# Kernel tuning notes

Hardware: AMD Instinct MI355X
Metric: run time of the kernel (lower is better)

Reference implementation:

```python
import jax, jax.numpy as jnp
import numpy as np

N, IN_CH, OUT_CH, E = 16384, 512, 512, 8


def setup_inputs() -> dict:
    key = jax.random.key(0)
    k1, k2, k3, k4 = jax.random.split(key, 4)
    x = jax.random.normal(k1, (N, IN_CH), dtype=jnp.float32)
    coefficients = jax.random.uniform(k2, (N, E), dtype=jnp.float32)
    # kaiming-uniform-ish init: bound = 1/sqrt(fan_in)
    bound = 1.0 / np.sqrt(IN_CH)
    weight = jax.random.uniform(k3, (E, OUT_CH, IN_CH), minval=-bound, maxval=bound, dtype=jnp.float32)
    bias = jax.random.uniform(k4, (E, OUT_CH), minval=-bound, maxval=bound, dtype=jnp.float32)
    return {"x": x, "coefficients": coefficients, "weight": weight, "bias": bias}


def reference(x, coefficients, weight, bias):
    # Original: mixed_weight = einsum('bc,cmn->bmn', coef, W); out = baddbmm(mixed_bias, mixed_weight, x)
    # Equivalent (by bilinearity) without materializing the (N,out,in) tensor:
    # per-expert matvec combined with coefficients in one einsum.
    out = jnp.einsum('ne,eoi,ni->no', coefficients, weight, x)
    out = out + coefficients @ bias  # (N,E) @ (E,out) -> (N,out)
    return out
```

## Files before the change

### kernel.cpp

```cpp
#include <hip/hip_runtime.h>

#define N_TOK 16384
#define CIN   512
#define COUT  512
#define NE    8
#define BM    256
#define BN    128
#define BK    64
#define KTILES 64

typedef __attribute__((ext_vector_type(8))) short bf16x8;
typedef __attribute__((ext_vector_type(4))) short s16x4;
typedef __attribute__((ext_vector_type(4))) float f32x4;

__device__ __forceinline__ short f2bf(float f) {
  unsigned u = __builtin_bit_cast(unsigned, f);
  u += 0x7FFFu + ((u >> 16) & 1u);
  return (short)(u >> 16);
}

__global__ void cvt_all(const float4* __restrict__ x, const float4* __restrict__ w,
                        s16x4* __restrict__ xb, s16x4* __restrict__ wb) {
  int i = blockIdx.x * blockDim.x + threadIdx.x;
  const int NX = N_TOK * CIN / 4;
  float4 v; s16x4* o;
  if (i < NX) { v = x[i]; o = xb + i; }
  else       { int j = i - NX; v = w[j]; o = wb + j; }
  s16x4 r;
  r[0] = f2bf(v.x); r[1] = f2bf(v.y); r[2] = f2bf(v.z); r[3] = f2bf(v.w);
  *o = r;
}

__device__ __forceinline__ void async16(short* lds, const short* g) {
  __builtin_amdgcn_global_load_lds(
      (const __attribute__((address_space(1))) void*)g,
      (__attribute__((address_space(3))) void*)lds, 16, 0, 0);
}

__global__ __launch_bounds__(512, 2)
void moe_gemm(const short* __restrict__ xb,
              const short* __restrict__ wb,
              const float* __restrict__ coef,
              const float* __restrict__ bias,
              float* __restrict__ out) {
  __shared__ short As[2][BM * BK];
  __shared__ short Bs[2][BN * BK];
  __shared__ float cfc[BM * NE];
  __shared__ float cfr[BM * NE];

  const int tid  = threadIdx.x;
  const int lane = tid & 63;
  const int wid  = tid >> 6;
  const int wm   = wid >> 1;
  const int wn   = wid & 1;
  const int lhi  = lane >> 4;
  const int llo  = lane & 15;

  const int bid0 = blockIdx.x;
  const int bid  = (bid0 & 7) * 32 + (bid0 >> 3);
  const int ct   = bid & 3;
  const int rt   = bid >> 2;
  const int row0 = rt * BM;
  const int col0 = ct * BN;

  ((float4*)cfc)[tid] = ((const float4*)(coef + row0 * NE))[tid];

  const int r_st = tid >> 3;
  const int c_sw = ((tid & 7) * 8) ^ ((r_st & 7) << 3);
  const short* gA = xb + (size_t)(row0 + r_st) * CIN + c_sw;
  const short* gB = wb + (size_t)(col0 + r_st) * CIN + c_sw;

  auto stage = [&](int buf, int t) {
    const int e  = t >> 3;
    const int i0 = (t & 7) * BK;
#pragma unroll
    for (int p = 0; p < 4; ++p)
      async16(&As[buf][p * 4096 + tid * 8], gA + p * 64 * CIN + i0);
#pragma unroll
    for (int p = 0; p < 2; ++p)
      async16(&Bs[buf][p * 4096 + tid * 8], gB + (size_t)e * (CIN * COUT) + p * 64 * CIN + i0);
  };

  stage(0, 0);
  asm volatile("s_waitcnt lgkmcnt(0)");
  __builtin_amdgcn_s_barrier();
  if (tid < BM) {
    const float* cp = &cfc[tid * NE];
    float c[NE];
#pragma unroll
    for (int e = 0; e < NE; ++e) c[e] = fmaxf(cp[e], 1e-20f);
    float* rp = &cfr[tid * NE];
#pragma unroll
    for (int e = 0; e < NE - 1; ++e) rp[e] = c[e] / c[e + 1];
    rp[NE - 1] = c[NE - 1];
  }
  asm volatile("s_waitcnt vmcnt(0) lgkmcnt(0)");
  __builtin_amdgcn_s_barrier();

  const int swz0 = (lhi * 8) ^ ((llo & 7) << 3);
  const int swz1 = (32 + lhi * 8) ^ ((llo & 7) << 3);
  const int arow = wm * 64 + llo;
  const int brow = wn * 64 + llo;

  f32x4 acc[4][4];
#pragma unroll
  for (int m = 0; m < 4; ++m)
#pragma unroll
    for (int n = 0; n < 4; ++n)
      acc[m][n] = (f32x4){0.f, 0.f, 0.f, 0.f};

  for (int t = 0; t < KTILES; ++t) {
    const int cur = t & 1;
    const short* Ab = As[cur];
    const short* Bb = Bs[cur];

    if (t + 1 < KTILES) stage(cur ^ 1, t + 1);
    bf16x8 bf[4][2];
#pragma unroll
    for (int n = 0; n < 4; ++n) {
      bf[n][0] = *(const bf16x8*)&Bb[(brow + n * 16) * 64 + swz0];
      bf[n][1] = *(const bf16x8*)&Bb[(brow + n * 16) * 64 + swz1];
    }
    bf16x8 af[2][2];
#pragma unroll
    for (int mm = 0; mm < 2; ++mm) {
      af[mm][0] = *(const bf16x8*)&Ab[(arow + mm * 16) * 64 + swz0];
      af[mm][1] = *(const bf16x8*)&Ab[(arow + mm * 16) * 64 + swz1];
    }
    __builtin_amdgcn_s_barrier();
    asm volatile("s_waitcnt lgkmcnt(0)");
    __builtin_amdgcn_s_setprio(1);
#pragma unroll
    for (int mm = 0; mm < 2; ++mm)
#pragma unroll
      for (int n = 0; n < 4; ++n)
#pragma unroll
        for (int ks = 0; ks < 2; ++ks)
          acc[mm][n] = __builtin_amdgcn_mfma_f32_16x16x32_bf16(
              af[mm][ks], bf[n][ks], acc[mm][n], 0, 0, 0);
    __builtin_amdgcn_s_setprio(0);
    __builtin_amdgcn_s_barrier();

#pragma unroll
    for (int mm = 0; mm < 2; ++mm) {
      af[mm][0] = *(const bf16x8*)&Ab[(arow + (2 + mm) * 16) * 64 + swz0];
      af[mm][1] = *(const bf16x8*)&Ab[(arow + (2 + mm) * 16) * 64 + swz1];
    }
    __builtin_amdgcn_s_barrier();
    asm volatile("s_waitcnt lgkmcnt(0)");
    __builtin_amdgcn_s_setprio(1);
#pragma unroll
    for (int mm = 0; mm < 2; ++mm)
#pragma unroll
      for (int n = 0; n < 4; ++n)
#pragma unroll
        for (int ks = 0; ks < 2; ++ks)
          acc[2 + mm][n] = __builtin_amdgcn_mfma_f32_16x16x32_bf16(
              af[mm][ks], bf[n][ks], acc[2 + mm][n], 0, 0, 0);
    __builtin_amdgcn_s_setprio(0);
    __builtin_amdgcn_s_barrier();

    if ((t & 7) == 7) {
      const int e = t >> 3;
#pragma unroll
      for (int m = 0; m < 4; ++m)
#pragma unroll
        for (int r = 0; r < 4; ++r) {
          float rr = cfr[(wm * 64 + m * 16 + lhi * 4 + r) * NE + e];
#pragma unroll
          for (int n = 0; n < 4; ++n)
            acc[m][n][r] *= rr;
        }
    }

    if (t + 1 < KTILES) {
      asm volatile("s_waitcnt vmcnt(0)");
      __builtin_amdgcn_s_barrier();
    }
  }

  float bcol[4][NE];
#pragma unroll
  for (int n = 0; n < 4; ++n) {
    const int cg = col0 + wn * 64 + n * 16 + llo;
#pragma unroll
    for (int e = 0; e < NE; ++e) bcol[n][e] = bias[e * COUT + cg];
  }
#pragma unroll
  for (int m = 0; m < 4; ++m)
#pragma unroll
    for (int r = 0; r < 4; ++r) {
      const int rl = wm * 64 + m * 16 + lhi * 4 + r;
      float cv[NE];
#pragma unroll
      for (int e = 0; e < NE; ++e) cv[e] = cfc[rl * NE + e];
      float* orow = out + (size_t)(row0 + rl) * COUT;
#pragma unroll
      for (int n = 0; n < 4; ++n) {
        float bm = 0.f;
#pragma unroll
        for (int e = 0; e < NE; ++e) bm += cv[e] * bcol[n][e];
        orow[col0 + wn * 64 + n * 16 + llo] = acc[m][n][r] + bm;
      }
    }
}

extern "C" void kernel_launch(void* const* d_in, const int* in_sizes, int n_in,
                              void* d_out, int out_size, void* d_ws, size_t ws_size,
                              hipStream_t stream) {
  const float* x    = (const float*)d_in[0];
  const float* coef = (const float*)d_in[1];
  const float* w    = (const float*)d_in[2];
  const float* bias = (const float*)d_in[3];
  float* out = (float*)d_out;

  short* xb = (short*)d_ws;
  short* wb = xb + (size_t)N_TOK * CIN;

  const int NX = N_TOK * CIN / 4, NW = NE * COUT * CIN / 4;
  cvt_all<<<(NX + NW) / 256, 256, 0, stream>>>(
      (const float4*)x, (const float4*)w, (s16x4*)xb, (s16x4*)wb);

  moe_gemm<<<(N_TOK / BM) * (COUT / BN), 512, 0, stream>>>(xb, wb, coef, bias, out);
}
```

Before: 183.6 us.

## Load A fragments straight to registers, halve row tile, grid-stride convert

The GEMM block shrinks to 128 rows with 256 threads. The activation (A) operand no longer goes through LDS: each wave loads its bf16 MFMA fragments straight from global memory into registers, double-buffered one tile ahead. Only the weight tile is staged through LDS with async loads, which removes the A LDS traffic and most intra-tile barriers. In exchange, A rows are fetched twice, once by each column wave, with no LDS reuse, and global latency must be hidden by the register prefetch. The conversion kernel also becomes a fixed 2048-block grid-stride loop.

Result: slower. 227.1 us (+23.7%).

```diff
diff --git a/kernel.cpp b/kernel.cpp
--- a/kernel.cpp
+++ b/kernel.cpp
@@ -4,7 +4,7 @@
 #define CIN   512
 #define COUT  512
 #define NE    8
-#define BM    256
+#define BM    128
 #define BN    128
 #define BK    64
 #define KTILES 64
@@ -21,14 +21,16 @@
 
 __global__ void cvt_all(const float4* __restrict__ x, const float4* __restrict__ w,
                         s16x4* __restrict__ xb, s16x4* __restrict__ wb) {
-  int i = blockIdx.x * blockDim.x + threadIdx.x;
   const int NX = N_TOK * CIN / 4;
-  float4 v; s16x4* o;
-  if (i < NX) { v = x[i]; o = xb + i; }
-  else       { int j = i - NX; v = w[j]; o = wb + j; }
-  s16x4 r;
-  r[0] = f2bf(v.x); r[1] = f2bf(v.y); r[2] = f2bf(v.z); r[3] = f2bf(v.w);
-  *o = r;
+  const int NT = NX + NE * COUT * CIN / 4;
+  for (int i = blockIdx.x * blockDim.x + threadIdx.x; i < NT; i += gridDim.x * blockDim.x) {
+    float4 v; s16x4* o;
+    if (i < NX) { v = x[i]; o = xb + i; }
+    else        { int j = i - NX; v = w[j]; o = wb + j; }
+    s16x4 r;
+    r[0] = f2bf(v.x); r[1] = f2bf(v.y); r[2] = f2bf(v.z); r[3] = f2bf(v.w);
+    *o = r;
+  }
 }
 
 __device__ __forceinline__ void async16(short* lds, const short* g) {
@@ -37,13 +39,12 @@
       (__attribute__((address_space(3))) void*)lds, 16, 0, 0);
 }
 
-__global__ __launch_bounds__(512, 2)
+__global__ __launch_bounds__(256, 2)
 void moe_gemm(const short* __restrict__ xb,
               const short* __restrict__ wb,
               const float* __restrict__ coef,
               const float* __restrict__ bias,
               float* __restrict__ out) {
-  __shared__ short As[2][BM * BK];
   __shared__ short Bs[2][BN * BK];
   __shared__ float cfc[BM * NE];
   __shared__ float cfr[BM * NE];
@@ -57,9 +58,10 @@
   const int llo  = lane & 15;
 
   const int bid0 = blockIdx.x;
-  const int bid  = (bid0 & 7) * 32 + (bid0 >> 3);
-  const int ct   = bid & 3;
-  const int rt   = bid >> 2;
+  const int xx   = bid0 & 7;
+  const int jj   = bid0 >> 3;
+  const int rt   = (xx >> 2) * 64 + jj;
+  const int ct   = xx & 3;
   const int row0 = rt * BM;
   const int col0 = ct * BN;
 
@@ -67,23 +69,43 @@
 
   const int r_st = tid >> 3;
   const int c_sw = ((tid & 7) * 8) ^ ((r_st & 7) << 3);
-  const short* gA = xb + (size_t)(row0 + r_st) * CIN + c_sw;
   const short* gB = wb + (size_t)(col0 + r_st) * CIN + c_sw;
 
-  auto stage = [&](int buf, int t) {
+  auto stageB = [&](int buf, int t) {
     const int e  = t >> 3;
     const int i0 = (t & 7) * BK;
 #pragma unroll
     for (int p = 0; p < 4; ++p)
-      async16(&As[buf][p * 4096 + tid * 8], gA + p * 64 * CIN + i0);
-#pragma unroll
-    for (int p = 0; p < 2; ++p)
-      async16(&Bs[buf][p * 4096 + tid * 8], gB + (size_t)e * (CIN * COUT) + p * 64 * CIN + i0);
+      async16(&Bs[buf][p * 2048 + tid * 8],
+              gB + (size_t)e * (CIN * COUT) + p * 32 * CIN + i0);
   };
 
-  stage(0, 0);
-  asm volatile("s_waitcnt lgkmcnt(0)");
-  __builtin_amdgcn_s_barrier();
+  const short* gA = xb + (size_t)(row0 + wm * 64 + llo) * CIN + lhi * 8;
+  auto loadA = [&](bf16x8 dst[4][2], int t) {
+    const int i0 = (t & 7) * 64;
+#pragma unroll
+    for (int m = 0; m < 4; ++m)
+#pragma unroll
+      for (int ks = 0; ks < 2; ++ks)
+        dst[m][ks] = *(const bf16x8*)(gA + (size_t)m * 16 * CIN + i0 + ks * 32);
+  };
+
+  const int swz0 = (lhi * 8) ^ ((llo & 7) << 3);
+  const int swz1 = (32 + lhi * 8) ^ ((llo & 7) << 3);
+  const int brow = wn * 64 + llo;
+
+  f32x4 acc[4][4];
+#pragma unroll
+  for (int m = 0; m < 4; ++m)
+#pragma unroll
+    for (int n = 0; n < 4; ++n)
+      acc[m][n] = (f32x4){0.f, 0.f, 0.f, 0.f};
+
+  bf16x8 af0[4][2], af1[4][2];
+
+  stageB(0, 0);
+  loadA(af0, 0);
+  __syncthreads();
   if (tid < BM) {
     const float* cp = &cfc[tid * NE];
     float c[NE];
@@ -94,71 +116,31 @@
     for (int e = 0; e < NE - 1; ++e) rp[e] = c[e] / c[e + 1];
     rp[NE - 1] = c[NE - 1];
   }
-  asm volatile("s_waitcnt vmcnt(0) lgkmcnt(0)");
-  __builtin_amdgcn_s_barrier();
-
-  const int swz0 = (lhi * 8) ^ ((llo & 7) << 3);
-  const int swz1 = (32 + lhi * 8) ^ ((llo & 7) << 3);
-  const int arow = wm * 64 + llo;
-  const int brow = wn * 64 + llo;
-
-  f32x4 acc[4][4];
-#pragma unroll
-  for (int m = 0; m < 4; ++m)
-#pragma unroll
-    for (int n = 0; n < 4; ++n)
-      acc[m][n] = (f32x4){0.f, 0.f, 0.f, 0.f};
-
-  for (int t = 0; t < KTILES; ++t) {
-    const int cur = t & 1;
-    const short* Ab = As[cur];
-    const short* Bb = Bs[cur];
-
-    if (t + 1 < KTILES) stage(cur ^ 1, t + 1);
+  __syncthreads();
+
+  auto tilebody = [&](bf16x8 (&cur)[4][2], bf16x8 (&nxt)[4][2], int t) {
+    const int buf = t & 1;
+    if (t + 1 < KTILES) {
+      loadA(nxt, t + 1);
+      stageB(buf ^ 1, t + 1);
+    }
+    const short* Bb = Bs[buf];
     bf16x8 bf[4][2];
 #pragma unroll
     for (int n = 0; n < 4; ++n) {
       bf[n][0] = *(const bf16x8*)&Bb[(brow + n * 16) * 64 + swz0];
       bf[n][1] = *(const bf16x8*)&Bb[(brow + n * 16) * 64 + swz1];
     }
-    bf16x8 af[2][2];
-#pragma unroll
-    for (int mm = 0; mm < 2; ++mm) {
-      af[mm][0] = *(const bf16x8*)&Ab[(arow + mm * 16) * 64 + swz0];
-      af[mm][1] = *(const bf16x8*)&Ab[(arow + mm * 16) * 64 + swz1];
-    }
-    __builtin_amdgcn_s_barrier();
-    asm volatile("s_waitcnt lgkmcnt(0)");
     __builtin_amdgcn_s_setprio(1);
 #pragma unroll
-    for (int mm = 0; mm < 2; ++mm)
+    for (int m = 0; m < 4; ++m)
 #pragma unroll
       for (int n = 0; n < 4; ++n)
 #pragma unroll
         for (int ks = 0; ks < 2; ++ks)
-          acc[mm][n] = __builtin_amdgcn_mfma_f32_16x16x32_bf16(
-              af[mm][ks], bf[n][ks], acc[mm][n], 0, 0, 0);
+          acc[m][n] = __builtin_amdgcn_mfma_f32_16x16x32_bf16(
+              cur[m][ks], bf[n][ks], acc[m][n], 0, 0, 0);
     __builtin_amdgcn_s_setprio(0);
-    __builtin_amdgcn_s_barrier();
-
-#pragma unroll
-    for (int mm = 0; mm < 2; ++mm) {
-      af[mm][0] = *(const bf16x8*)&Ab[(arow + (2 + mm) * 16) * 64 + swz0];
-      af[mm][1] = *(const bf16x8*)&Ab[(arow + (2 + mm) * 16) * 64 + swz1];
-    }
-    __builtin_amdgcn_s_barrier();
-    asm volatile("s_waitcnt lgkmcnt(0)");
-    __builtin_amdgcn_s_setprio(1);
-#pragma unroll
-    for (int mm = 0; mm < 2; ++mm)
-#pragma unroll
-      for (int n = 0; n < 4; ++n)
-#pragma unroll
-        for (int ks = 0; ks < 2; ++ks)
-          acc[2 + mm][n] = __builtin_amdgcn_mfma_f32_16x16x32_bf16(
-              af[mm][ks], bf[n][ks], acc[2 + mm][n], 0, 0, 0);
-    __builtin_amdgcn_s_setprio(0);
-    __builtin_amdgcn_s_barrier();
 
     if ((t & 7) == 7) {
       const int e = t >> 3;
@@ -173,10 +155,12 @@
         }
     }
 
-    if (t + 1 < KTILES) {
-      asm volatile("s_waitcnt vmcnt(0)");
-      __builtin_amdgcn_s_barrier();
-    }
+    if (t + 1 < KTILES) __syncthreads();
+  };
+
+  for (int t = 0; t < KTILES; t += 2) {
+    tilebody(af0, af1, t);
+    tilebody(af1, af0, t + 1);
   }
 
   float bcol[4][NE];
@@ -217,9 +201,8 @@
   short* xb = (short*)d_ws;
   short* wb = xb + (size_t)N_TOK * CIN;
 
-  const int NX = N_TOK * CIN / 4, NW = NE * COUT * CIN / 4;
-  cvt_all<<<(NX + NW) / 256, 256, 0, stream>>>(
+  cvt_all<<<2048, 256, 0, stream>>>(
       (const float4*)x, (const float4*)w, (s16x4*)xb, (s16x4*)wb);
 
-  moe_gemm<<<(N_TOK / BM) * (COUT / BN), 512, 0, stream>>>(xb, wb, coef, bias, out);
-}
+  moe_gemm<<<(N_TOK / BM) * (COUT / BN), 256, 0, stream>>>(xb, wb, coef, bias, out);
+}
```

## Triple-buffer GEMM tiles, fold bias into rescale chain, grid-stride conversion

Applied to the files above, without the earlier changes.

The GEMM main loop moves from double to triple LDS buffering with a prefetch distance of two tiles. A and B staging is split across the two MFMA halves, and the per-iteration full vmcnt(0) wait becomes a partial vmcnt(6) wait, with sched_barriers pinning instruction order. Bias is now folded into the per-expert ratio rescale chain, and coefficients are read straight from global, which removes the epilogue bias matmul and one LDS array. The block-to-tile mapping and the conversion kernel grid (now a fixed-size grid-stride loop) also change. This raises LDS use (three buffers plus a bias tile), which may limit blocks per CU, and relies on the vmcnt count matching the in-flight loads.

Measured after the change: 183.6 us. No clear change (+0.0%).

```diff
diff --git a/kernel.cpp b/kernel.cpp
--- a/kernel.cpp
+++ b/kernel.cpp
@@ -21,14 +21,16 @@
 
 __global__ void cvt_all(const float4* __restrict__ x, const float4* __restrict__ w,
                         s16x4* __restrict__ xb, s16x4* __restrict__ wb) {
-  int i = blockIdx.x * blockDim.x + threadIdx.x;
   const int NX = N_TOK * CIN / 4;
-  float4 v; s16x4* o;
-  if (i < NX) { v = x[i]; o = xb + i; }
-  else       { int j = i - NX; v = w[j]; o = wb + j; }
-  s16x4 r;
-  r[0] = f2bf(v.x); r[1] = f2bf(v.y); r[2] = f2bf(v.z); r[3] = f2bf(v.w);
-  *o = r;
+  const int NT = NX + NE * COUT * CIN / 4;
+  for (int i = blockIdx.x * blockDim.x + threadIdx.x; i < NT; i += gridDim.x * blockDim.x) {
+    float4 v; s16x4* o;
+    if (i < NX) { v = x[i]; o = xb + i; }
+    else        { int j = i - NX; v = w[j]; o = wb + j; }
+    s16x4 r;
+    r[0] = f2bf(v.x); r[1] = f2bf(v.y); r[2] = f2bf(v.z); r[3] = f2bf(v.w);
+    *o = r;
+  }
 }
 
 __device__ __forceinline__ void async16(short* lds, const short* g) {
@@ -36,6 +38,11 @@
       (const __attribute__((address_space(1))) void*)g,
       (__attribute__((address_space(3))) void*)lds, 16, 0, 0);
 }
+
+#define SBAR()  do { __builtin_amdgcn_sched_barrier(0); __builtin_amdgcn_s_barrier(); \
+                     __builtin_amdgcn_sched_barrier(0); } while (0)
+#define WAIT_LGKM0() do { asm volatile("s_waitcnt lgkmcnt(0)" ::: "memory"); \
+                          __builtin_amdgcn_sched_barrier(0); } while (0)
 
 __global__ __launch_bounds__(512, 2)
 void moe_gemm(const short* __restrict__ xb,
@@ -43,10 +50,10 @@
               const float* __restrict__ coef,
               const float* __restrict__ bias,
               float* __restrict__ out) {
-  __shared__ short As[2][BM * BK];
-  __shared__ short Bs[2][BN * BK];
-  __shared__ float cfc[BM * NE];
+  __shared__ short As[3][BM * BK];
+  __shared__ short Bs[3][BN * BK];
   __shared__ float cfr[BM * NE];
+  __shared__ float bb[NE * BN];
 
   const int tid  = threadIdx.x;
   const int lane = tid & 63;
@@ -57,45 +64,51 @@
   const int llo  = lane & 15;
 
   const int bid0 = blockIdx.x;
-  const int bid  = (bid0 & 7) * 32 + (bid0 >> 3);
-  const int ct   = bid & 3;
-  const int rt   = bid >> 2;
+  const int xx   = bid0 & 7;
+  const int jj   = bid0 >> 3;
+  const int rt   = (xx >> 2) * 32 + jj;
+  const int ct   = xx & 3;
   const int row0 = rt * BM;
   const int col0 = ct * BN;
-
-  ((float4*)cfc)[tid] = ((const float4*)(coef + row0 * NE))[tid];
 
   const int r_st = tid >> 3;
   const int c_sw = ((tid & 7) * 8) ^ ((r_st & 7) << 3);
   const short* gA = xb + (size_t)(row0 + r_st) * CIN + c_sw;
   const short* gB = wb + (size_t)(col0 + r_st) * CIN + c_sw;
 
-  auto stage = [&](int buf, int t) {
+  auto stageA = [&](int buf, int t) {
+    const int i0 = (t & 7) * BK;
+#pragma unroll
+    for (int p = 0; p < 4; ++p)
+      async16(&As[buf][p * 4096 + tid * 8], gA + p * 64 * CIN + i0);
+  };
+  auto stageB = [&](int buf, int t) {
     const int e  = t >> 3;
     const int i0 = (t & 7) * BK;
 #pragma unroll
-    for (int p = 0; p < 4; ++p)
-      async16(&As[buf][p * 4096 + tid * 8], gA + p * 64 * CIN + i0);
-#pragma unroll
     for (int p = 0; p < 2; ++p)
-      async16(&Bs[buf][p * 4096 + tid * 8], gB + (size_t)e * (CIN * COUT) + p * 64 * CIN + i0);
+      async16(&Bs[buf][p * 4096 + tid * 8],
+              gB + (size_t)e * (CIN * COUT) + p * 64 * CIN + i0);
   };
 
-  stage(0, 0);
-  asm volatile("s_waitcnt lgkmcnt(0)");
-  __builtin_amdgcn_s_barrier();
+  if (tid < 256) {
+    const int e = tid >> 5, c4 = tid & 31;
+    ((float4*)bb)[tid] = ((const float4*)(bias + e * COUT + col0))[c4];
+  }
   if (tid < BM) {
-    const float* cp = &cfc[tid * NE];
-    float c[NE];
-#pragma unroll
-    for (int e = 0; e < NE; ++e) c[e] = fmaxf(cp[e], 1e-20f);
+    const float4* cp = (const float4*)(coef + (size_t)(row0 + tid) * NE);
+    float4 cl = cp[0], ch = cp[1];
+    float c[NE] = {cl.x, cl.y, cl.z, cl.w, ch.x, ch.y, ch.z, ch.w};
+#pragma unroll
+    for (int e = 0; e < NE; ++e) c[e] = fmaxf(c[e], 1e-20f);
     float* rp = &cfr[tid * NE];
 #pragma unroll
     for (int e = 0; e < NE - 1; ++e) rp[e] = c[e] / c[e + 1];
     rp[NE - 1] = c[NE - 1];
   }
-  asm volatile("s_waitcnt vmcnt(0) lgkmcnt(0)");
-  __builtin_amdgcn_s_barrier();
+  stageA(0, 0); stageB(0, 0);
+  stageA(1, 1); stageB(1, 1);
+  __syncthreads();
 
   const int swz0 = (lhi * 8) ^ ((llo & 7) << 3);
   const int swz1 = (32 + lhi * 8) ^ ((llo & 7) << 3);
@@ -109,26 +122,27 @@
     for (int n = 0; n < 4; ++n)
       acc[m][n] = (f32x4){0.f, 0.f, 0.f, 0.f};
 
+  int cur = 0;
   for (int t = 0; t < KTILES; ++t) {
-    const int cur = t & 1;
+    const int nx2 = (cur < 1) ? cur + 2 : cur - 1;
     const short* Ab = As[cur];
     const short* Bb = Bs[cur];
-
-    if (t + 1 < KTILES) stage(cur ^ 1, t + 1);
-    bf16x8 bf[4][2];
+    const bool pf = (t + 2) < KTILES;
+
+    if (pf) stageA(nx2, t + 2);
+    bf16x8 af[2][2], bf[4][2];
 #pragma unroll
     for (int n = 0; n < 4; ++n) {
       bf[n][0] = *(const bf16x8*)&Bb[(brow + n * 16) * 64 + swz0];
       bf[n][1] = *(const bf16x8*)&Bb[(brow + n * 16) * 64 + swz1];
     }
-    bf16x8 af[2][2];
 #pragma unroll
     for (int mm = 0; mm < 2; ++mm) {
       af[mm][0] = *(const bf16x8*)&Ab[(arow + mm * 16) * 64 + swz0];
       af[mm][1] = *(const bf16x8*)&Ab[(arow + mm * 16) * 64 + swz1];
     }
-    __builtin_amdgcn_s_barrier();
-    asm volatile("s_waitcnt lgkmcnt(0)");
+    SBAR();
+    WAIT_LGKM0();
     __builtin_amdgcn_s_setprio(1);
 #pragma unroll
     for (int mm = 0; mm < 2; ++mm)
@@ -139,15 +153,16 @@
           acc[mm][n] = __builtin_amdgcn_mfma_f32_16x16x32_bf16(
               af[mm][ks], bf[n][ks], acc[mm][n], 0, 0, 0);
     __builtin_amdgcn_s_setprio(0);
-    __builtin_amdgcn_s_barrier();
-
+    SBAR();
+
+    if (pf) stageB(nx2, t + 2);
 #pragma unroll
     for (int mm = 0; mm < 2; ++mm) {
       af[mm][0] = *(const bf16x8*)&Ab[(arow + (2 + mm) * 16) * 64 + swz0];
       af[mm][1] = *(const bf16x8*)&Ab[(arow + (2 + mm) * 16) * 64 + swz1];
     }
-    __builtin_amdgcn_s_barrier();
-    asm volatile("s_waitcnt lgkmcnt(0)");
+    SBAR();
+    WAIT_LGKM0();
     __builtin_amdgcn_s_setprio(1);
 #pragma unroll
     for (int mm = 0; mm < 2; ++mm)
@@ -158,10 +173,12 @@
           acc[2 + mm][n] = __builtin_amdgcn_mfma_f32_16x16x32_bf16(
               af[mm][ks], bf[n][ks], acc[2 + mm][n], 0, 0, 0);
     __builtin_amdgcn_s_setprio(0);
-    __builtin_amdgcn_s_barrier();
 
     if ((t & 7) == 7) {
       const int e = t >> 3;
+      float bv[4];
+#pragma unroll
+      for (int n = 0; n < 4; ++n) bv[n] = bb[e * BN + wn * 64 + n * 16 + llo];
 #pragma unroll
       for (int m = 0; m < 4; ++m)
 #pragma unroll
@@ -169,39 +186,31 @@
           float rr = cfr[(wm * 64 + m * 16 + lhi * 4 + r) * NE + e];
 #pragma unroll
           for (int n = 0; n < 4; ++n)
-            acc[m][n][r] *= rr;
+            acc[m][n][r] = (acc[m][n][r] + bv[n]) * rr;
         }
     }
 
-    if (t + 1 < KTILES) {
-      asm volatile("s_waitcnt vmcnt(0)");
-      __builtin_amdgcn_s_barrier();
-    }
-  }
-
-  float bcol[4][NE];
-#pragma unroll
-  for (int n = 0; n < 4; ++n) {
-    const int cg = col0 + wn * 64 + n * 16 + llo;
-#pragma unroll
-    for (int e = 0; e < NE; ++e) bcol[n][e] = bias[e * COUT + cg];
-  }
+    if (pf) {
+      asm volatile("s_waitcnt vmcnt(6)" ::: "memory");
+      __builtin_amdgcn_sched_barrier(0);
+      SBAR();
+    } else if (t + 1 < KTILES) {
+      asm volatile("s_waitcnt vmcnt(0)" ::: "memory");
+      __builtin_amdgcn_sched_barrier(0);
+      SBAR();
+    }
+    cur = (cur == 2) ? 0 : cur + 1;
+  }
+
 #pragma unroll
   for (int m = 0; m < 4; ++m)
 #pragma unroll
     for (int r = 0; r < 4; ++r) {
       const int rl = wm * 64 + m * 16 + lhi * 4 + r;
-      float cv[NE];
-#pragma unroll
-      for (int e = 0; e < NE; ++e) cv[e] = cfc[rl * NE + e];
       float* orow = out + (size_t)(row0 + rl) * COUT;
 #pragma unroll
-      for (int n = 0; n < 4; ++n) {
-        float bm = 0.f;
-#pragma unroll
-        for (int e = 0; e < NE; ++e) bm += cv[e] * bcol[n][e];
-        orow[col0 + wn * 64 + n * 16 + llo] = acc[m][n][r] + bm;
-      }
+      for (int n = 0; n < 4; ++n)
+        orow[col0 + wn * 64 + n * 16 + llo] = acc[m][n][r];
     }
 }
 
@@ -217,8 +226,7 @@
   short* xb = (short*)d_ws;
   short* wb = xb + (size_t)N_TOK * CIN;
 
-  const int NX = N_TOK * CIN / 4, NW = NE * COUT * CIN / 4;
-  cvt_all<<<(NX + NW) / 256, 256, 0, stream>>>(
+  cvt_all<<<2048, 256, 0, stream>>>(
       (const float4*)x, (const float4*)w, (s16x4*)xb, (s16x4*)wb);
 
   moe_gemm<<<(N_TOK / BM) * (COUT / BN), 512, 0, stream>>>(xb, wb, coef, bias, out);
```
